# Kernel tuning notes

Measured on AMD Instinct MI355X. Metric: run time of the kernel, lower is better.

## Reference

```python
import jax, jax.numpy as jnp
import numpy as np

# LocBlock.get_obj_matrix, fully vectorized over batch B and points N.
# Per point i: Q_e[c,c]=w_i*kron(m_i m_i^T, I3), Q_e[t,t]=w_i*I3,
# Q_e[h,h]=w_i*y_i^T y_i, Q_e[c,t]=-w_i*kron(m_i, I3), Q_e[c,h]=-w_i*kron(m_i, y_i),
# Q_e[t,h]=w_i*y_i; summed over i, then offset removed and Frobenius-normalized.

B, N = 1024, 4096

def setup_inputs() -> dict:
    key = jax.random.key(0)
    k1, k2, k3 = jax.random.split(key, 3)
    return {
        "keypoints_3D_src": jax.random.normal(k1, (B, 3, N), dtype=jnp.float32),
        "keypoints_3D_trg": jax.random.normal(k2, (B, 3, N), dtype=jnp.float32),
        "weights": jax.random.uniform(k3, (B, 1, N), dtype=jnp.float32),
    }


def reference(keypoints_3D_src, keypoints_3D_trg, weights):
    m = keypoints_3D_src              # (B,3,N) source points
    y = keypoints_3D_trg              # (B,3,N) target points
    w = weights[:, 0, :]              # (B,N) per-point scalar weights
    b = m.shape[0]
    I3 = jnp.eye(3, dtype=m.dtype)

    # weighted moment sums over points
    Mw = jnp.einsum('bin,bjn,bn->bij', m, m, w)          # (B,3,3) sum w m m^T
    mw = jnp.einsum('bin,bn->bi', m, w)                  # (B,3)   sum w m
    yw = jnp.einsum('bin,bn->bi', y, w)                  # (B,3)   sum w y
    MY = jnp.einsum('bin,bjn,bn->bij', m, y, w)          # (B,3,3) sum w m y^T
    sw = jnp.sum(w, axis=-1)                             # (B,)    sum w
    yy = jnp.einsum('bin,bin,bn->b', y, y, w)            # (B,)    sum w y^T y

    # assemble blocks (kron index convention: kron(A,B)[3i+k,3j+l]=A[ij]B[kl])
    Qcc = jnp.einsum('bij,kl->bikjl', Mw, I3).reshape(b, 9, 9)   # kron(Mw, I3)
    Qct = -jnp.einsum('bi,kl->bikl', mw, I3).reshape(b, 9, 3)    # -kron(mw, I3)
    Qch = -MY.reshape(b, 9)                                      # -kron(m, W y) summed
    Qtt = sw[:, None, None] * I3                                 # (B,3,3)

    Q = jnp.zeros((b, 13, 13), dtype=m.dtype)
    Q = Q.at[:, 1:10, 1:10].set(Qcc)
    Q = Q.at[:, 10:13, 10:13].set(Qtt)
    Q = Q.at[:, 1:10, 10:13].set(Qct)
    Q = Q.at[:, 10:13, 1:10].set(jnp.swapaxes(Qct, 1, 2))
    Q = Q.at[:, 1:10, 0].set(Qch)
    Q = Q.at[:, 0, 1:10].set(Qch)
    Q = Q.at[:, 10:13, 0].set(yw)
    Q = Q.at[:, 0, 10:13].set(yw)
    # Q[0,0] would be yy (offset); original zeroes it before normalization
    offsets = yy
    scales = jnp.sqrt(jnp.sum(Q * Q, axis=(1, 2)))  # Frobenius norm with Q[0,0]=0
    Qn = Q / scales[:, None, None]
    return Qn, scales, offsets
```

## Files before the change

### kernel.cpp

```cpp
#include <hip/hip_runtime.h>
#include <math.h>

#define BATCH    1024
#define NPTS     4096
#define THREADS  256
#define WAVES    (THREADS / 64)
#define NV       (NPTS / 4)
#define ITERS    (NV / THREADS)
#define NACC     23
#define RPAD     264

typedef float fx4 __attribute__((ext_vector_type(4)));


__global__ __launch_bounds__(THREADS, 3) void locblock_fused(
    const float* __restrict__ m,
    const float* __restrict__ y,
    const float* __restrict__ w,
    float* __restrict__ out)
{
    const int b    = blockIdx.x;
    const int tid  = threadIdx.x;
    const int lane = tid & 63;
    const int wave = tid >> 6;

    const size_t mb = (size_t)b * 3 * NPTS;
    const float* m0p = m + mb + 0 * NPTS;
    const float* m1p = m + mb + 1 * NPTS;
    const float* m2p = m + mb + 2 * NPTS;
    const float* y0p = y + mb + 0 * NPTS;
    const float* y1p = y + mb + 1 * NPTS;
    const float* y2p = y + mb + 2 * NPTS;
    const float* wp  = w + (size_t)b * NPTS;

    fx4 M0[ITERS], M1[ITERS], M2[ITERS], Y0[ITERS], Y1[ITERS], Y2[ITERS], W[ITERS];
#pragma unroll
    for (int it = 0; it < ITERS; ++it) {
        const int v = (it * THREADS + tid) * 4;
        M0[it] = *(const fx4*)(m0p + v);
        M1[it] = *(const fx4*)(m1p + v);
        M2[it] = *(const fx4*)(m2p + v);
        Y0[it] = *(const fx4*)(y0p + v);
        Y1[it] = *(const fx4*)(y1p + v);
        Y2[it] = *(const fx4*)(y2p + v);
        W[it]  = *(const fx4*)(wp  + v);
    }

    float acc[NACC];
#pragma unroll
    for (int i = 0; i < NACC; ++i) acc[i] = 0.f;

    auto accum = [&](float wv, float m0v, float m1v, float m2v,
                     float y0v, float y1v, float y2v) {
        float wm0 = wv * m0v, wm1 = wv * m1v, wm2 = wv * m2v;
        acc[0]  += wv;
        acc[1]  += wm0;        acc[2]  += wm1;        acc[3]  += wm2;
        acc[4]  += wv * y0v;   acc[5]  += wv * y1v;   acc[6]  += wv * y2v;
        acc[7]  += wm0 * m0v;  acc[8]  += wm0 * m1v;  acc[9]  += wm0 * m2v;
        acc[10] += wm1 * m1v;  acc[11] += wm1 * m2v;  acc[12] += wm2 * m2v;
        acc[13] += wm0 * y0v;  acc[14] += wm0 * y1v;  acc[15] += wm0 * y2v;
        acc[16] += wm1 * y0v;  acc[17] += wm1 * y1v;  acc[18] += wm1 * y2v;
        acc[19] += wm2 * y0v;  acc[20] += wm2 * y1v;  acc[21] += wm2 * y2v;
        acc[22] += wv * (y0v * y0v + y1v * y1v + y2v * y2v);
    };

#pragma unroll
    for (int it = 0; it < ITERS; ++it) {
#pragma unroll
        for (int e = 0; e < 4; ++e) {
            accum(W[it][e], M0[it][e], M1[it][e], M2[it][e],
                  Y0[it][e], Y1[it][e], Y2[it][e]);
        }
    }

    __shared__ float red_lds[NACC * RPAD];
    __shared__ float sums[NACC];
    __shared__ float sqred[WAVES];
    __shared__ float scale_s;

#pragma unroll
    for (int i = 0; i < NACC; ++i) red_lds[i * RPAD + tid] = acc[i];
    __syncthreads();

    if (wave == 0) {
        float part[NACC];
#pragma unroll
        for (int i = 0; i < NACC; ++i) {
            const float* row = &red_lds[i * RPAD + lane];
            part[i] = row[0] + row[64] + row[128] + row[192];
        }
#pragma unroll
        for (int i = 0; i < NACC; ++i) {
            float v = part[i];
            v += __shfl_xor(v, 32, 64);
            v += __shfl_xor(v, 16, 64);
            v += __shfl_xor(v, 8, 64);
            v += __shfl_xor(v, 4, 64);
            v += __shfl_xor(v, 2, 64);
            v += __shfl_xor(v, 1, 64);
            part[i] = v;
        }
        if (lane == 0) {
#pragma unroll
            for (int i = 0; i < NACC; ++i) sums[i] = part[i];
        }
    }
    __syncthreads();

    float qv = 0.f;
    if (tid < 169) {
        const int r = tid / 13, c = tid % 13;
        const float* mwv = &sums[1];
        const float* ywv = &sums[4];
        auto Mwf = [&](int i, int j) -> float {
            if (i > j) { int t = i; i = j; j = t; }
            int idx = (i == 0) ? j : ((i == 1) ? (j + 2) : 5);
            return sums[7 + idx];
        };
        auto MYf = [&](int i, int j) -> float { return sums[13 + i * 3 + j]; };

        if (r == 0) {
            if (c == 0)            qv = 0.f;
            else if (c <= 9)       qv = -MYf((c - 1) / 3, (c - 1) % 3);
            else                   qv = ywv[c - 10];
        } else if (c == 0) {
            if (r <= 9)            qv = -MYf((r - 1) / 3, (r - 1) % 3);
            else                   qv = ywv[r - 10];
        } else if (r <= 9 && c <= 9) {
            int a = r - 1, d = c - 1;
            int i = a / 3, k = a % 3, j = d / 3, l = d % 3;
            qv = (k == l) ? Mwf(i, j) : 0.f;
        } else if (r <= 9) {
            int a = r - 1, i = a / 3, k = a % 3, l = c - 10;
            qv = (k == l) ? -mwv[i] : 0.f;
        } else if (c <= 9) {
            int a = c - 1, i = a / 3, k = a % 3, l = r - 10;
            qv = (k == l) ? -mwv[i] : 0.f;
        } else {
            qv = (r == c) ? sums[0] : 0.f;
        }
    }

    float sq = (tid < 169) ? qv * qv : 0.f;
    sq += __shfl_xor(sq, 32, 64);
    sq += __shfl_xor(sq, 16, 64);
    sq += __shfl_xor(sq, 8, 64);
    sq += __shfl_xor(sq, 4, 64);
    sq += __shfl_xor(sq, 2, 64);
    sq += __shfl_xor(sq, 1, 64);
    if (lane == 0) sqred[wave] = sq;
    __syncthreads();
    if (tid == 0) {
        scale_s = sqrtf(sqred[0] + sqred[1] + sqred[2] + sqred[3]);
    }
    __syncthreads();

    const float inv_scale = 1.0f / scale_s;
    if (tid < 169) {
        out[(size_t)b * 169 + tid] = qv * inv_scale;
    }
    if (tid == 0) {
        out[(size_t)BATCH * 169 + b]         = scale_s;
        out[(size_t)BATCH * 169 + BATCH + b] = sums[22];
    }
}

extern "C" void kernel_launch(void* const* d_in, const int* in_sizes, int n_in,
                              void* d_out, int out_size, void* d_ws, size_t ws_size,
                              hipStream_t stream) {
    const float* m = (const float*)d_in[0];
    const float* y = (const float*)d_in[1];
    const float* w = (const float*)d_in[2];
    float* out = (float*)d_out;
    locblock_fused<<<BATCH, THREADS, 0, stream>>>(m, y, w, out);
}
```

Baseline: 137.6 us.

## Stage inputs through LDS with direct global-to-LDS loads in two halves

Replaces the per-thread register loads of all 28 float4 values with global_load_lds transfers into a 56KB shared buffer, processed in two halves of the point range. The shared buffer is reused for the reduction scratch. The aim is to cut register pressure and use the direct async load path. In exchange, the large LDS footprint limits blocks per CU, it adds barriers, and the two halves are serialized with no overlap between loading and computing.

```diff
diff --git a/kernel.cpp b/kernel.cpp
--- a/kernel.cpp
+++ b/kernel.cpp
@@ -4,16 +4,17 @@
 #define BATCH    1024
 #define NPTS     4096
 #define THREADS  256
-#define WAVES    (THREADS / 64)
-#define NV       (NPTS / 4)
-#define ITERS    (NV / THREADS)
+#define WAVES    4
+#define HALF     (NPTS / 2)
+#define NSTREAM  7
+#define CHUNKS   8
 #define NACC     23
 #define RPAD     264
 
 typedef float fx4 __attribute__((ext_vector_type(4)));
 
 
-__global__ __launch_bounds__(THREADS, 3) void locblock_fused(
+__global__ __launch_bounds__(THREADS) void locblock_fused(
     const float* __restrict__ m,
     const float* __restrict__ y,
     const float* __restrict__ w,
@@ -25,26 +26,16 @@
     const int wave = tid >> 6;
 
     const size_t mb = (size_t)b * 3 * NPTS;
-    const float* m0p = m + mb + 0 * NPTS;
-    const float* m1p = m + mb + 1 * NPTS;
-    const float* m2p = m + mb + 2 * NPTS;
-    const float* y0p = y + mb + 0 * NPTS;
-    const float* y1p = y + mb + 1 * NPTS;
-    const float* y2p = y + mb + 2 * NPTS;
-    const float* wp  = w + (size_t)b * NPTS;
+    const float* rows[NSTREAM] = {
+        m + mb + 0 * NPTS, m + mb + 1 * NPTS, m + mb + 2 * NPTS,
+        y + mb + 0 * NPTS, y + mb + 1 * NPTS, y + mb + 2 * NPTS,
+        w + (size_t)b * NPTS
+    };
 
-    fx4 M0[ITERS], M1[ITERS], M2[ITERS], Y0[ITERS], Y1[ITERS], Y2[ITERS], W[ITERS];
-#pragma unroll
-    for (int it = 0; it < ITERS; ++it) {
-        const int v = (it * THREADS + tid) * 4;
-        M0[it] = *(const fx4*)(m0p + v);
-        M1[it] = *(const fx4*)(m1p + v);
-        M2[it] = *(const fx4*)(m2p + v);
-        Y0[it] = *(const fx4*)(y0p + v);
-        Y1[it] = *(const fx4*)(y1p + v);
-        Y2[it] = *(const fx4*)(y2p + v);
-        W[it]  = *(const fx4*)(wp  + v);
-    }
+    __shared__ float smem[NSTREAM * HALF];
+    __shared__ float sums[NACC];
+    __shared__ float sqred[WAVES];
+    __shared__ float scale_s;
 
     float acc[NACC];
 #pragma unroll
@@ -64,29 +55,49 @@
         acc[22] += wv * (y0v * y0v + y1v * y1v + y2v * y2v);
     };
 
+    for (int h = 0; h < 2; ++h) {
 #pragma unroll
-    for (int it = 0; it < ITERS; ++it) {
+        for (int s = 0; s < NSTREAM; ++s) {
 #pragma unroll
-        for (int e = 0; e < 4; ++e) {
-            accum(W[it][e], M0[it][e], M1[it][e], M2[it][e],
-                  Y0[it][e], Y1[it][e], Y2[it][e]);
+            for (int k = 0; k < 2; ++k) {
+                const int c = wave * 2 + k;
+                const float* g = rows[s] + h * HALF + c * 256 + lane * 4;
+                float* l = &smem[s * HALF + c * 256];
+                __builtin_amdgcn_global_load_lds(
+                    (__attribute__((address_space(1))) void*)(float*)g,
+                    (__attribute__((address_space(3))) void*)l,
+                    16, 0, 0);
+            }
         }
+        __syncthreads();
+
+#pragma unroll
+        for (int k = 0; k < 2; ++k) {
+            const int idx = (k * THREADS + tid) * 4;
+            fx4 vm0 = *(const fx4*)&smem[0 * HALF + idx];
+            fx4 vm1 = *(const fx4*)&smem[1 * HALF + idx];
+            fx4 vm2 = *(const fx4*)&smem[2 * HALF + idx];
+            fx4 vy0 = *(const fx4*)&smem[3 * HALF + idx];
+            fx4 vy1 = *(const fx4*)&smem[4 * HALF + idx];
+            fx4 vy2 = *(const fx4*)&smem[5 * HALF + idx];
+            fx4 vw  = *(const fx4*)&smem[6 * HALF + idx];
+#pragma unroll
+            for (int e = 0; e < 4; ++e) {
+                accum(vw[e], vm0[e], vm1[e], vm2[e], vy0[e], vy1[e], vy2[e]);
+            }
+        }
+        __syncthreads();
     }
 
-    __shared__ float red_lds[NACC * RPAD];
-    __shared__ float sums[NACC];
-    __shared__ float sqred[WAVES];
-    __shared__ float scale_s;
-
 #pragma unroll
-    for (int i = 0; i < NACC; ++i) red_lds[i * RPAD + tid] = acc[i];
+    for (int i = 0; i < NACC; ++i) smem[i * RPAD + tid] = acc[i];
     __syncthreads();
 
     if (wave == 0) {
         float part[NACC];
 #pragma unroll
         for (int i = 0; i < NACC; ++i) {
-            const float* row = &red_lds[i * RPAD + lane];
+            const float* row = &smem[i * RPAD + lane];
             part[i] = row[0] + row[64] + row[128] + row[192];
         }
 #pragma unroll
```

Result: no change. 137.2 us (-0.3%).
